# Performance work log

Measured on AMD Instinct MI355X. Metric: run time of the kernel, lower is better.

## Reference

```python
import jax, jax.numpy as jnp
import numpy as np

B, S, HID = 2, 2048, 768
NH, HD = 12, 64  # num heads, head dim


def setup_inputs() -> dict:
    key = jax.random.key(0)
    ks = jax.random.split(key, 10)
    scale = 0.02
    return {
        "hidden_states": jax.random.normal(ks[0], (B, S, HID), jnp.float32),
        "rel_pos": jax.random.normal(ks[1], (B, NH, S, S), jnp.float32),
        "rel_2d_pos": jax.random.normal(ks[2], (B, NH, S, S), jnp.float32),
        "attention_mask": jax.random.randint(ks[3], (B, 1, S, S), 0, 2, jnp.int32),
        "Wq": jax.random.normal(ks[4], (HID, HID), jnp.float32) * scale,
        "bq": jnp.zeros((HID,), jnp.float32),
        "Wk": jax.random.normal(ks[5], (HID, HID), jnp.float32) * scale,
        "bk": jnp.zeros((HID,), jnp.float32),
        "Wv": jax.random.normal(ks[6], (HID, HID), jnp.float32) * scale,
        "bv": jnp.zeros((HID,), jnp.float32),
    }


def _heads(x):
    # [B,S,HID] -> [B,NH,S,HD]
    return x.reshape(B, S, NH, HD).transpose(0, 2, 1, 3)


def reference(hidden_states, rel_pos, rel_2d_pos, attention_mask, Wq, bq, Wk, bk, Wv, bv):
    q = _heads(hidden_states @ Wq.T + bq) / jnp.sqrt(jnp.asarray(HD, hidden_states.dtype))
    k = _heads(hidden_states @ Wk.T + bk)
    v = _heads(hidden_states @ Wv.T + bv)
    scores = jnp.einsum('bhsd,bhtd->bhst', q, k)
    scores = scores + rel_pos + rel_2d_pos
    scores = jnp.where(attention_mask.astype(bool), jnp.finfo(jnp.float32).min, scores.astype(jnp.float32))
    probs = jax.nn.softmax(scores, axis=-1).astype(v.dtype)
    ctx = jnp.einsum('bhst,bhtd->bhsd', probs, v)
    return ctx.transpose(0, 2, 1, 3).reshape(B, S, HID)
```

## Files before the change

### kernel.cpp

```cpp
#include <hip/hip_runtime.h>

#define B_ 2
#define S_ 2048
#define HID_ 768
#define NH_ 12
#define HD_ 64
#define NSPLIT 2
#define KSPAN (S_ / NSPLIT)
#define NROWS (B_ * NH_ * S_)

typedef unsigned short u16;
typedef __attribute__((ext_vector_type(8))) short bf16x8;
typedef __attribute__((ext_vector_type(4))) float f32x4;

static __device__ inline u16 f2bf(float f) {
    union { float f; unsigned u; } v; v.f = f;
    unsigned r = v.u + 0x7fffu + ((v.u >> 16) & 1u);
    return (u16)(r >> 16);
}

#define LDS_BARRIER() asm volatile("s_waitcnt lgkmcnt(0)\n\ts_barrier" ::: "memory")

__global__ void cast_bf16(const float* __restrict__ src, u16* __restrict__ dst, int n) {
    int i = (blockIdx.x * blockDim.x + threadIdx.x) * 4;
    if (i < n) {
        float4 v = *(const float4*)(src + i);
        unsigned lo = (unsigned)f2bf(v.x) | ((unsigned)f2bf(v.y) << 16);
        unsigned hi = (unsigned)f2bf(v.z) | ((unsigned)f2bf(v.w) << 16);
        uint2 o; o.x = lo; o.y = hi;
        *(uint2*)(dst + i) = o;
    }
}

__global__ __launch_bounds__(256) void qkv_gemm(
    const u16* __restrict__ hsb, const u16* __restrict__ wcat,
    const float* __restrict__ bq, const float* __restrict__ bk, const float* __restrict__ bv,
    u16* __restrict__ Qg, u16* __restrict__ Kg, u16* __restrict__ Vtg)
{
    __shared__ u16 As[64 * 40];
    __shared__ u16 Bs[64 * 40];
    __shared__ u16 Vs[64 * 72];

    const int m0 = blockIdx.x * 64;
    const int n0 = blockIdx.y * 64;
    const int tid = threadIdx.x;
    const int wave = tid >> 6, lane = tid & 63;
    const int l = lane & 15, quad = lane >> 4;

    f32x4 acc[4];
#pragma unroll
    for (int t = 0; t < 4; t++) acc[t] = (f32x4){0.f, 0.f, 0.f, 0.f};

    const int srow = tid >> 2;
    const int skg = (tid & 3) * 8;

    for (int k0 = 0; k0 < HID_; k0 += 32) {
        *(int4*)(&As[srow * 40 + skg]) = *(const int4*)(&hsb[(size_t)(m0 + srow) * HID_ + k0 + skg]);
        *(int4*)(&Bs[srow * 40 + skg]) = *(const int4*)(&wcat[(size_t)(n0 + srow) * HID_ + k0 + skg]);
        __syncthreads();
        bf16x8 a = *(const bf16x8*)(&As[(wave * 16 + l) * 40 + quad * 8]);
#pragma unroll
        for (int t = 0; t < 4; t++) {
            bf16x8 b = *(const bf16x8*)(&Bs[(t * 16 + l) * 40 + quad * 8]);
            acc[t] = __builtin_amdgcn_mfma_f32_16x16x32_bf16(a, b, acc[t], 0, 0, 0);
        }
        __syncthreads();
    }

    const int proj = n0 / HID_;
    const int cbase = n0 - proj * HID_;
    const int h = cbase >> 6;
    const int bidx = m0 >> 11;
    const int srow0 = m0 & (S_ - 1);
    const float* bias = (proj == 0) ? bq : ((proj == 1) ? bk : bv);

    if (proj < 2) {
        u16* dst = (proj == 0) ? Qg : Kg;
        const float sc = (proj == 0) ? 0.125f : 1.0f;
#pragma unroll
        for (int t = 0; t < 4; t++) {
            const int d = t * 16 + l;
            const float bb = bias[cbase + d];
#pragma unroll
            for (int rr = 0; rr < 4; rr++) {
                int s = srow0 + wave * 16 + quad * 4 + rr;
                float v = (acc[t][rr] + bb) * sc;
                dst[(((size_t)bidx * NH_ + h) * S_ + s) * HD_ + d] = f2bf(v);
            }
        }
    } else {
#pragma unroll
        for (int t = 0; t < 4; t++) {
            const int d = t * 16 + l;
            const float bb = bias[cbase + d];
#pragma unroll
            for (int rr = 0; rr < 4; rr++) {
                int sl = wave * 16 + quad * 4 + rr;
                Vs[d * 72 + sl] = f2bf(acc[t][rr] + bb);
            }
        }
        __syncthreads();
        const int drow = tid >> 2;
        const int sseg = (tid & 3) * 16;
        size_t base = (((size_t)bidx * NH_ + h) * HD_ + drow) * S_ + srow0 + sseg;
        *(int4*)(&Vtg[base])     = *(const int4*)(&Vs[drow * 72 + sseg]);
        *(int4*)(&Vtg[base + 8]) = *(const int4*)(&Vs[drow * 72 + sseg + 8]);
    }
}

__global__ __launch_bounds__(256) void attn(
    const u16* __restrict__ Qg, const u16* __restrict__ Kg, const u16* __restrict__ Vtg,
    const float* __restrict__ rel, const float* __restrict__ rel2,
    const int* __restrict__ mask,
    float* __restrict__ Opart, float* __restrict__ Mpart, float* __restrict__ Lpart)
{
    __shared__ u16 Ks[64 * 72];
    __shared__ u16 Vts[64 * 72];
    __shared__ u16 Ps[4 * 16 * 72];

    const int q0 = blockIdx.x * 64;
    const int h = blockIdx.y;
    const int b = blockIdx.z / NSPLIT;
    const int split = blockIdx.z - b * NSPLIT;
    const int tid = threadIdx.x;
    const int wave = tid >> 6, lane = tid & 63;
    const int l = lane & 15, quad = lane >> 4;
    const int bh = b * NH_ + h;
    const int kbase = split * KSPAN;
    const int kend = kbase + KSPAN;

    const float NEG = -3.4028234663852886e38f;

    bf16x8 qf[2];
    {
        const int qr = q0 + wave * 16 + l;
        qf[0] = *(const bf16x8*)(&Qg[((size_t)bh * S_ + qr) * HD_ + quad * 8]);
        qf[1] = *(const bf16x8*)(&Qg[((size_t)bh * S_ + qr) * HD_ + 32 + quad * 8]);
    }

    f32x4 o[4];
#pragma unroll
    for (int t = 0; t < 4; t++) o[t] = (f32x4){0.f, 0.f, 0.f, 0.f};
    float m_run = NEG, l_run = 0.f;

    const int srow = tid >> 2;
    const int sseg = (tid & 3) * 8;

    const int qrow = q0 + wave * 16 + l;
    const float* relR  = rel  + (size_t)bh * S_ * S_ + (size_t)qrow * S_;
    const float* rel2R = rel2 + (size_t)bh * S_ * S_ + (size_t)qrow * S_;
    const int*   maskR = mask + (size_t)b * S_ * S_ + (size_t)qrow * S_;

    float4 pr1[4], pr2[4];
    int4 pmk[4];
#pragma unroll
    for (int t = 0; t < 4; t++) {
        const int c = kbase + t * 16 + quad * 4;
        pr1[t] = *(const float4*)(relR + c);
        pr2[t] = *(const float4*)(rel2R + c);
        pmk[t] = *(const int4*)(maskR + c);
    }

    for (int k0 = kbase; k0 < kend; k0 += 64) {
        size_t kg = ((size_t)bh * S_ + k0 + srow) * HD_;
        int4 ka = *(const int4*)(&Kg[kg + sseg]);
        int4 kb = *(const int4*)(&Kg[kg + 32 + sseg]);
        size_t vg = ((size_t)bh * HD_ + srow) * S_ + k0;
        int4 va = *(const int4*)(&Vtg[vg + sseg]);
        int4 vb = *(const int4*)(&Vtg[vg + 32 + sseg]);

        f32x4 sacc[4];
#pragma unroll
        for (int t = 0; t < 4; t++) {
            sacc[t][0] = pmk[t].x ? NEG : pr1[t].x + pr2[t].x;
            sacc[t][1] = pmk[t].y ? NEG : pr1[t].y + pr2[t].y;
            sacc[t][2] = pmk[t].z ? NEG : pr1[t].z + pr2[t].z;
            sacc[t][3] = pmk[t].w ? NEG : pr1[t].w + pr2[t].w;
        }

        if (k0 + 64 < kend) {
#pragma unroll
            for (int t = 0; t < 4; t++) {
                const int c = k0 + 64 + t * 16 + quad * 4;
                pr1[t] = *(const float4*)(relR + c);
                pr2[t] = *(const float4*)(rel2R + c);
                pmk[t] = *(const int4*)(maskR + c);
            }
        }

        *(int4*)(&Ks[srow * 72 + sseg])       = ka;
        *(int4*)(&Ks[srow * 72 + 32 + sseg])  = kb;
        *(int4*)(&Vts[srow * 72 + sseg])      = va;
        *(int4*)(&Vts[srow * 72 + 32 + sseg]) = vb;
        LDS_BARRIER();

#pragma unroll
        for (int t = 0; t < 4; t++) {
            bf16x8 b0 = *(const bf16x8*)(&Ks[(t * 16 + l) * 72 + quad * 8]);
            sacc[t] = __builtin_amdgcn_mfma_f32_16x16x32_bf16(b0, qf[0], sacc[t], 0, 0, 0);
            bf16x8 b1 = *(const bf16x8*)(&Ks[(t * 16 + l) * 72 + 32 + quad * 8]);
            sacc[t] = __builtin_amdgcn_mfma_f32_16x16x32_bf16(b1, qf[1], sacc[t], 0, 0, 0);
        }

        float mx = NEG;
#pragma unroll
        for (int t = 0; t < 4; t++)
#pragma unroll
            for (int rr = 0; rr < 4; rr++) mx = fmaxf(mx, sacc[t][rr]);
        mx = fmaxf(mx, __shfl_xor(mx, 16, 64));
        mx = fmaxf(mx, __shfl_xor(mx, 32, 64));
        float mnew = fmaxf(m_run, mx);
        float alpha = __expf(m_run - mnew);
        float rs = 0.f;
#pragma unroll
        for (int t = 0; t < 4; t++)
#pragma unroll
            for (int rr = 0; rr < 4; rr++) {
                float p = __expf(sacc[t][rr] - mnew);
                sacc[t][rr] = p;
                rs += p;
            }
        rs += __shfl_xor(rs, 16, 64);
        rs += __shfl_xor(rs, 32, 64);
        l_run = l_run * alpha + rs;
        m_run = mnew;

        float av[4];
#pragma unroll
        for (int rr = 0; rr < 4; rr++) av[rr] = __shfl(alpha, quad * 4 + rr, 64);
#pragma unroll
        for (int dt = 0; dt < 4; dt++)
#pragma unroll
            for (int rr = 0; rr < 4; rr++) o[dt][rr] *= av[rr];

#pragma unroll
        for (int t = 0; t < 4; t++) {
            unsigned p01 = (unsigned)f2bf(sacc[t][0]) | ((unsigned)f2bf(sacc[t][1]) << 16);
            unsigned p23 = (unsigned)f2bf(sacc[t][2]) | ((unsigned)f2bf(sacc[t][3]) << 16);
            uint2 pw; pw.x = p01; pw.y = p23;
            *(uint2*)(&Ps[(wave * 16 + l) * 72 + t * 16 + quad * 4]) = pw;
        }

        bf16x8 pa0 = *(const bf16x8*)(&Ps[(wave * 16 + l) * 72 + quad * 8]);
        bf16x8 pa1 = *(const bf16x8*)(&Ps[(wave * 16 + l) * 72 + 32 + quad * 8]);
#pragma unroll
        for (int dt = 0; dt < 4; dt++) {
            bf16x8 v0 = *(const bf16x8*)(&Vts[(dt * 16 + l) * 72 + quad * 8]);
            o[dt] = __builtin_amdgcn_mfma_f32_16x16x32_bf16(pa0, v0, o[dt], 0, 0, 0);
            bf16x8 v1 = *(const bf16x8*)(&Vts[(dt * 16 + l) * 72 + 32 + quad * 8]);
            o[dt] = __builtin_amdgcn_mfma_f32_16x16x32_bf16(pa1, v1, o[dt], 0, 0, 0);
        }
        LDS_BARRIER();
    }

    float* Op = Opart + (((size_t)split * B_ * NH_ + bh) * S_ + q0) * HD_;
#pragma unroll
    for (int dt = 0; dt < 4; dt++) {
#pragma unroll
        for (int rr = 0; rr < 4; rr++) {
            const int row = wave * 16 + quad * 4 + rr;
            Op[(size_t)row * HD_ + dt * 16 + l] = o[dt][rr];
        }
    }
    if (quad == 0) {
        const size_t mi = ((size_t)split * B_ * NH_ + bh) * S_ + q0 + wave * 16 + l;
        Mpart[mi] = m_run;
        Lpart[mi] = l_run;
    }
}

__global__ __launch_bounds__(256) void combine(
    const float* __restrict__ Op, const float* __restrict__ Mp, const float* __restrict__ Lp,
    float* __restrict__ out)
{
    const int idx = blockIdx.x * 256 + threadIdx.x;
    const int r = idx >> 4;
    const int dseg = (idx & 15) * 4;
    const float m0 = Mp[r], m1 = Mp[NROWS + r];
    const float l0 = Lp[r], l1 = Lp[NROWS + r];
    const float m = fmaxf(m0, m1);
    const float a0 = __expf(m0 - m), a1 = __expf(m1 - m);
    const float inv = 1.0f / (l0 * a0 + l1 * a1);
    const float4 o0 = *(const float4*)(Op + (size_t)r * HD_ + dseg);
    const float4 o1 = *(const float4*)(Op + ((size_t)NROWS + r) * HD_ + dseg);
    float4 res;
    res.x = (o0.x * a0 + o1.x * a1) * inv;
    res.y = (o0.y * a0 + o1.y * a1) * inv;
    res.z = (o0.z * a0 + o1.z * a1) * inv;
    res.w = (o0.w * a0 + o1.w * a1) * inv;
    const int bh_ = r >> 11;
    const int s = r & (S_ - 1);
    const int b = bh_ / NH_;
    const int h = bh_ - b * NH_;
    *(float4*)(out + ((size_t)(b * S_ + s)) * HID_ + h * HD_ + dseg) = res;
}

extern "C" void kernel_launch(void* const* d_in, const int* in_sizes, int n_in,
                              void* d_out, int out_size, void* d_ws, size_t ws_size,
                              hipStream_t stream) {
    const float* hs   = (const float*)d_in[0];
    const float* rel  = (const float*)d_in[1];
    const float* rel2 = (const float*)d_in[2];
    const int*   mask = (const int*)d_in[3];
    const float* Wq = (const float*)d_in[4];
    const float* bq = (const float*)d_in[5];
    const float* Wk = (const float*)d_in[6];
    const float* bk = (const float*)d_in[7];
    const float* Wv = (const float*)d_in[8];
    const float* bv = (const float*)d_in[9];
    float* out = (float*)d_out;

    char* ws = (char*)d_ws;
    u16* hsb   = (u16*)(ws);
    u16* wcat  = (u16*)(ws + 6291456);
    u16* Qg    = (u16*)(ws + 9830400);
    u16* Kg    = (u16*)(ws + 16121856);
    u16* Vtg   = (u16*)(ws + 22413312);
    float* Opart = (float*)(ws + 28704768);
    float* Mpart = (float*)(ws + 53870592);
    float* Lpart = (float*)(ws + 54263808);

    cast_bf16<<<3072, 256, 0, stream>>>(hs, hsb, B_ * S_ * HID_);
    cast_bf16<<<576, 256, 0, stream>>>(Wq, wcat,             HID_ * HID_);
    cast_bf16<<<576, 256, 0, stream>>>(Wk, wcat + HID_ * HID_,     HID_ * HID_);
    cast_bf16<<<576, 256, 0, stream>>>(Wv, wcat + 2 * HID_ * HID_, HID_ * HID_);

    qkv_gemm<<<dim3(64, 36), 256, 0, stream>>>(hsb, wcat, bq, bk, bv, Qg, Kg, Vtg);

    attn<<<dim3(S_ / 64, NH_, B_ * NSPLIT), 256, 0, stream>>>(
        Qg, Kg, Vtg, rel, rel2, mask, Opart, Mpart, Lpart);

    combine<<<(NROWS * 16) / 256, 256, 0, stream>>>(Opart, Mpart, Lpart, out);
}
```

Measured before the change: 905.7 us.

## Coalesce rel_pos/mask loads by row-major lane mapping and redistribute via shuffles

Changes how each wave loads the rel_pos, rel_2d_pos and mask tiles. Each group of four lanes now reads a contiguous 64-element row segment, replacing the scattered per-lane row reads. The values are then moved into the MFMA accumulator layout with cross-lane shuffles. This also removes the register prefetch of the next tile, so the loads are issued in the same iteration and are exposed, in exchange for better coalescing and fewer live registers.

```diff
diff --git a/kernel.cpp b/kernel.cpp
--- a/kernel.cpp
+++ b/kernel.cpp
@@ -146,20 +146,13 @@
     const int srow = tid >> 2;
     const int sseg = (tid & 3) * 8;
 
-    const int qrow = q0 + wave * 16 + l;
-    const float* relR  = rel  + (size_t)bh * S_ * S_ + (size_t)qrow * S_;
-    const float* rel2R = rel2 + (size_t)bh * S_ * S_ + (size_t)qrow * S_;
-    const int*   maskR = mask + (size_t)b * S_ * S_ + (size_t)qrow * S_;
-
-    float4 pr1[4], pr2[4];
-    int4 pmk[4];
-#pragma unroll
-    for (int t = 0; t < 4; t++) {
-        const int c = kbase + t * 16 + quad * 4;
-        pr1[t] = *(const float4*)(relR + c);
-        pr2[t] = *(const float4*)(rel2R + c);
-        pmk[t] = *(const int4*)(maskR + c);
-    }
+    const int rsub = lane >> 2;
+    const int rcol = (lane & 3) * 4;
+    const int rrow = q0 + wave * 16 + rsub;
+    const float* relS  = rel  + (size_t)bh * S_ * S_ + (size_t)rrow * S_;
+    const float* rel2S = rel2 + (size_t)bh * S_ * S_ + (size_t)rrow * S_;
+    const int*   maskS = mask + (size_t)b  * S_ * S_ + (size_t)rrow * S_;
+    const int srcLane = 4 * l + quad;
 
     for (int k0 = kbase; k0 < kend; k0 += 64) {
         size_t kg = ((size_t)bh * S_ + k0 + srow) * HD_;
@@ -169,29 +162,39 @@
         int4 va = *(const int4*)(&Vtg[vg + sseg]);
         int4 vb = *(const int4*)(&Vtg[vg + 32 + sseg]);
 
-        f32x4 sacc[4];
-#pragma unroll
-        for (int t = 0; t < 4; t++) {
-            sacc[t][0] = pmk[t].x ? NEG : pr1[t].x + pr2[t].x;
-            sacc[t][1] = pmk[t].y ? NEG : pr1[t].y + pr2[t].y;
-            sacc[t][2] = pmk[t].z ? NEG : pr1[t].z + pr2[t].z;
-            sacc[t][3] = pmk[t].w ? NEG : pr1[t].w + pr2[t].w;
-        }
-
-        if (k0 + 64 < kend) {
-#pragma unroll
-            for (int t = 0; t < 4; t++) {
-                const int c = k0 + 64 + t * 16 + quad * 4;
-                pr1[t] = *(const float4*)(relR + c);
-                pr2[t] = *(const float4*)(rel2R + c);
-                pmk[t] = *(const int4*)(maskR + c);
-            }
+        float4 r[4], s2[4];
+        int4 mk[4];
+#pragma unroll
+        for (int i = 0; i < 4; i++) {
+            const int c = k0 + rcol + i * 16;
+            r[i]  = *(const float4*)(relS + c);
+            s2[i] = *(const float4*)(rel2S + c);
+            mk[i] = *(const int4*)(maskS + c);
         }
 
         *(int4*)(&Ks[srow * 72 + sseg])       = ka;
         *(int4*)(&Ks[srow * 72 + 32 + sseg])  = kb;
         *(int4*)(&Vts[srow * 72 + sseg])      = va;
         *(int4*)(&Vts[srow * 72 + 32 + sseg]) = vb;
+
+        f32x4 ss[4];
+#pragma unroll
+        for (int i = 0; i < 4; i++) {
+            ss[i][0] = mk[i].x ? NEG : r[i].x + s2[i].x;
+            ss[i][1] = mk[i].y ? NEG : r[i].y + s2[i].y;
+            ss[i][2] = mk[i].z ? NEG : r[i].z + s2[i].z;
+            ss[i][3] = mk[i].w ? NEG : r[i].w + s2[i].w;
+        }
+
+        f32x4 sacc[4];
+#pragma unroll
+        for (int t = 0; t < 4; t++) {
+            sacc[t][0] = __shfl(ss[t][0], srcLane, 64);
+            sacc[t][1] = __shfl(ss[t][1], srcLane, 64);
+            sacc[t][2] = __shfl(ss[t][2], srcLane, 64);
+            sacc[t][3] = __shfl(ss[t][3], srcLane, 64);
+        }
+
         LDS_BARRIER();
 
 #pragma unroll
```

Result: faster. 880.2 us (-2.8%).

## Bit-pack mask, stage rel-pos sums in LDS, shuffle P into MFMA operands

Applied to the files above, without the earlier changes.

A new pre-pass kernel packs the int32 attention mask into 64-bit ballot words, so the attention kernel reads one bit per element instead of an int32 per head. The attention kernel now loads rel_pos and rel_2d_pos with row-wise coalesced float4 loads in 256-column chunks. It adds them, applies the mask, and stores the result as bf16 in a large LDS buffer that each 64-key tile reads back. The P-to-MFMA-operand conversion now uses cross-lane shuffles instead of an LDS round trip. This is meant to cut global memory traffic and uncoalesced access, but the larger LDS footprint may lower occupancy and the bf16 bias sum adds rounding error.

```diff
diff --git a/kernel.cpp b/kernel.cpp
--- a/kernel.cpp
+++ b/kernel.cpp
@@ -10,6 +10,7 @@
 #define NROWS (B_ * NH_ * S_)
 
 typedef unsigned short u16;
+typedef unsigned int uint;
 typedef __attribute__((ext_vector_type(8))) short bf16x8;
 typedef __attribute__((ext_vector_type(4))) float f32x4;
 
@@ -17,6 +18,9 @@
     union { float f; unsigned u; } v; v.f = f;
     unsigned r = v.u + 0x7fffu + ((v.u >> 16) & 1u);
     return (u16)(r >> 16);
+}
+static __device__ inline float bf2f(uint u) {
+    union { unsigned u; float f; } v; v.u = u << 16; return v.f;
 }
 
 #define LDS_BARRIER() asm volatile("s_waitcnt lgkmcnt(0)\n\ts_barrier" ::: "memory")
@@ -32,6 +36,14 @@
     }
 }
 
+__global__ __launch_bounds__(256) void pack_mask(const int* __restrict__ m, uint2* __restrict__ out) {
+    const int w = blockIdx.x * 4 + (threadIdx.x >> 6);
+    const int lane = threadIdx.x & 63;
+    const int v = m[(size_t)w * 64 + lane];
+    unsigned long long bl = __ballot(v != 0);
+    if (lane == 0) { uint2 o; o.x = (uint)bl; o.y = (uint)(bl >> 32); out[w] = o; }
+}
+
 __global__ __launch_bounds__(256) void qkv_gemm(
     const u16* __restrict__ hsb, const u16* __restrict__ wcat,
     const float* __restrict__ bq, const float* __restrict__ bk, const float* __restrict__ bv,
@@ -111,12 +123,12 @@
 __global__ __launch_bounds__(256) void attn(
     const u16* __restrict__ Qg, const u16* __restrict__ Kg, const u16* __restrict__ Vtg,
     const float* __restrict__ rel, const float* __restrict__ rel2,
-    const int* __restrict__ mask,
+    const uint2* __restrict__ maskb,
     float* __restrict__ Opart, float* __restrict__ Mpart, float* __restrict__ Lpart)
 {
+    __shared__ u16 relsum[64 * 268];
     __shared__ u16 Ks[64 * 72];
     __shared__ u16 Vts[64 * 72];
-    __shared__ u16 Ps[4 * 16 * 72];
 
     const int q0 = blockIdx.x * 64;
     const int h = blockIdx.y;
@@ -127,15 +139,14 @@
     const int l = lane & 15, quad = lane >> 4;
     const int bh = b * NH_ + h;
     const int kbase = split * KSPAN;
-    const int kend = kbase + KSPAN;
 
     const float NEG = -3.4028234663852886e38f;
 
-    bf16x8 qf[2];
+    bf16x8 qf0, qf1;
     {
         const int qr = q0 + wave * 16 + l;
-        qf[0] = *(const bf16x8*)(&Qg[((size_t)bh * S_ + qr) * HD_ + quad * 8]);
-        qf[1] = *(const bf16x8*)(&Qg[((size_t)bh * S_ + qr) * HD_ + 32 + quad * 8]);
+        qf0 = *(const bf16x8*)(&Qg[((size_t)bh * S_ + qr) * HD_ + quad * 8]);
+        qf1 = *(const bf16x8*)(&Qg[((size_t)bh * S_ + qr) * HD_ + 32 + quad * 8]);
     }
 
     f32x4 o[4];
@@ -146,111 +157,142 @@
     const int srow = tid >> 2;
     const int sseg = (tid & 3) * 8;
 
-    const int qrow = q0 + wave * 16 + l;
-    const float* relR  = rel  + (size_t)bh * S_ * S_ + (size_t)qrow * S_;
-    const float* rel2R = rel2 + (size_t)bh * S_ * S_ + (size_t)qrow * S_;
-    const int*   maskR = mask + (size_t)b * S_ * S_ + (size_t)qrow * S_;
-
-    float4 pr1[4], pr2[4];
-    int4 pmk[4];
-#pragma unroll
-    for (int t = 0; t < 4; t++) {
-        const int c = kbase + t * 16 + quad * 4;
-        pr1[t] = *(const float4*)(relR + c);
-        pr2[t] = *(const float4*)(rel2R + c);
-        pmk[t] = *(const int4*)(maskR + c);
-    }
-
-    for (int k0 = kbase; k0 < kend; k0 += 64) {
-        size_t kg = ((size_t)bh * S_ + k0 + srow) * HD_;
-        int4 ka = *(const int4*)(&Kg[kg + sseg]);
-        int4 kb = *(const int4*)(&Kg[kg + 32 + sseg]);
-        size_t vg = ((size_t)bh * HD_ + srow) * S_ + k0;
-        int4 va = *(const int4*)(&Vtg[vg + sseg]);
-        int4 vb = *(const int4*)(&Vtg[vg + 32 + sseg]);
-
-        f32x4 sacc[4];
+    const float* relQ  = rel  + (size_t)bh * S_ * S_ + (size_t)q0 * S_;
+    const float* rel2Q = rel2 + (size_t)bh * S_ * S_ + (size_t)q0 * S_;
+    const uint2* mQ    = maskb + (size_t)(b * S_ + q0) * (S_ / 64);
+
+    const int A16a = l + 32 * (quad & 1);
+    const int A16b = A16a + 16;
+
+    for (int ss = 0; ss < KSPAN; ss += 256) {
+        const int c0 = kbase + ss;
+
+#pragma unroll
+        for (int g = 0; g < 2; g++) {
+            float4 xa[8], xb[8];
+            uint2  xm[8];
+#pragma unroll
+            for (int r = 0; r < 8; r++) {
+                const int rowl = wave * 16 + g * 8 + r;
+                xa[r] = *(const float4*)(relQ  + (size_t)rowl * S_ + c0 + 4 * lane);
+                xb[r] = *(const float4*)(rel2Q + (size_t)rowl * S_ + c0 + 4 * lane);
+                xm[r] = mQ[(size_t)rowl * (S_ / 64) + (c0 >> 6) + (lane >> 4)];
+            }
+#pragma unroll
+            for (int r = 0; r < 8; r++) {
+                const int rowl = wave * 16 + g * 8 + r;
+                const uint wsel = (lane & 8) ? xm[r].y : xm[r].x;
+                const uint nib = (wsel >> ((lane & 7) * 4)) & 0xF;
+                const u16 NEGB = (u16)0xFF7F;
+                u16 e0 = (nib & 1) ? NEGB : f2bf(xa[r].x + xb[r].x);
+                u16 e1 = (nib & 2) ? NEGB : f2bf(xa[r].y + xb[r].y);
+                u16 e2 = (nib & 4) ? NEGB : f2bf(xa[r].z + xb[r].z);
+                u16 e3 = (nib & 8) ? NEGB : f2bf(xa[r].w + xb[r].w);
+                uint2 pw; pw.x = (uint)e0 | ((uint)e1 << 16); pw.y = (uint)e2 | ((uint)e3 << 16);
+                *(uint2*)(&relsum[rowl * 268 + 4 * lane]) = pw;
+            }
+        }
+
 #pragma unroll
         for (int t = 0; t < 4; t++) {
-            sacc[t][0] = pmk[t].x ? NEG : pr1[t].x + pr2[t].x;
-            sacc[t][1] = pmk[t].y ? NEG : pr1[t].y + pr2[t].y;
-            sacc[t][2] = pmk[t].z ? NEG : pr1[t].z + pr2[t].z;
-            sacc[t][3] = pmk[t].w ? NEG : pr1[t].w + pr2[t].w;
-        }
-
-        if (k0 + 64 < kend) {
-#pragma unroll
-            for (int t = 0; t < 4; t++) {
-                const int c = k0 + 64 + t * 16 + quad * 4;
-                pr1[t] = *(const float4*)(relR + c);
-                pr2[t] = *(const float4*)(rel2R + c);
-                pmk[t] = *(const int4*)(maskR + c);
-            }
-        }
-
-        *(int4*)(&Ks[srow * 72 + sseg])       = ka;
-        *(int4*)(&Ks[srow * 72 + 32 + sseg])  = kb;
-        *(int4*)(&Vts[srow * 72 + sseg])      = va;
-        *(int4*)(&Vts[srow * 72 + 32 + sseg]) = vb;
-        LDS_BARRIER();
-
-#pragma unroll
-        for (int t = 0; t < 4; t++) {
-            bf16x8 b0 = *(const bf16x8*)(&Ks[(t * 16 + l) * 72 + quad * 8]);
-            sacc[t] = __builtin_amdgcn_mfma_f32_16x16x32_bf16(b0, qf[0], sacc[t], 0, 0, 0);
-            bf16x8 b1 = *(const bf16x8*)(&Ks[(t * 16 + l) * 72 + 32 + quad * 8]);
-            sacc[t] = __builtin_amdgcn_mfma_f32_16x16x32_bf16(b1, qf[1], sacc[t], 0, 0, 0);
-        }
-
-        float mx = NEG;
-#pragma unroll
-        for (int t = 0; t < 4; t++)
-#pragma unroll
-            for (int rr = 0; rr < 4; rr++) mx = fmaxf(mx, sacc[t][rr]);
-        mx = fmaxf(mx, __shfl_xor(mx, 16, 64));
-        mx = fmaxf(mx, __shfl_xor(mx, 32, 64));
-        float mnew = fmaxf(m_run, mx);
-        float alpha = __expf(m_run - mnew);
-        float rs = 0.f;
-#pragma unroll
-        for (int t = 0; t < 4; t++)
-#pragma unroll
-            for (int rr = 0; rr < 4; rr++) {
-                float p = __expf(sacc[t][rr] - mnew);
-                sacc[t][rr] = p;
-                rs += p;
-            }
-        rs += __shfl_xor(rs, 16, 64);
-        rs += __shfl_xor(rs, 32, 64);
-        l_run = l_run * alpha + rs;
-        m_run = mnew;
-
-        float av[4];
-#pragma unroll
-        for (int rr = 0; rr < 4; rr++) av[rr] = __shfl(alpha, quad * 4 + rr, 64);
-#pragma unroll
-        for (int dt = 0; dt < 4; dt++)
-#pragma unroll
-            for (int rr = 0; rr < 4; rr++) o[dt][rr] *= av[rr];
-
-#pragma unroll
-        for (int t = 0; t < 4; t++) {
-            unsigned p01 = (unsigned)f2bf(sacc[t][0]) | ((unsigned)f2bf(sacc[t][1]) << 16);
-            unsigned p23 = (unsigned)f2bf(sacc[t][2]) | ((unsigned)f2bf(sacc[t][3]) << 16);
-            uint2 pw; pw.x = p01; pw.y = p23;
-            *(uint2*)(&Ps[(wave * 16 + l) * 72 + t * 16 + quad * 4]) = pw;
-        }
-
-        bf16x8 pa0 = *(const bf16x8*)(&Ps[(wave * 16 + l) * 72 + quad * 8]);
-        bf16x8 pa1 = *(const bf16x8*)(&Ps[(wave * 16 + l) * 72 + 32 + quad * 8]);
-#pragma unroll
-        for (int dt = 0; dt < 4; dt++) {
-            bf16x8 v0 = *(const bf16x8*)(&Vts[(dt * 16 + l) * 72 + quad * 8]);
-            o[dt] = __builtin_amdgcn_mfma_f32_16x16x32_bf16(pa0, v0, o[dt], 0, 0, 0);
-            bf16x8 v1 = *(const bf16x8*)(&Vts[(dt * 16 + l) * 72 + 32 + quad * 8]);
-            o[dt] = __builtin_amdgcn_mfma_f32_16x16x32_bf16(pa1, v1, o[dt], 0, 0, 0);
-        }
-        LDS_BARRIER();
+            const int k0 = c0 + t * 64;
+
+            size_t kg = ((size_t)bh * S_ + k0 + srow) * HD_;
+            int4 ka = *(const int4*)(&Kg[kg + sseg]);
+            int4 kb = *(const int4*)(&Kg[kg + 32 + sseg]);
+            size_t vg = ((size_t)bh * HD_ + srow) * S_ + k0;
+            int4 va = *(const int4*)(&Vtg[vg + sseg]);
+            int4 vb = *(const int4*)(&Vtg[vg + 32 + sseg]);
+            *(int4*)(&Ks[srow * 72 + sseg])       = ka;
+            *(int4*)(&Ks[srow * 72 + 32 + sseg])  = kb;
+            *(int4*)(&Vts[srow * 72 + sseg])      = va;
+            *(int4*)(&Vts[srow * 72 + 32 + sseg]) = vb;
+            LDS_BARRIER();
+
+            f32x4 sacc[4];
+#pragma unroll
+            for (int tt = 0; tt < 4; tt++) {
+                uint2 rv = *(const uint2*)(&relsum[(wave * 16 + l) * 268 + ss - ss  + t * 64 + tt * 16 + quad * 4]);
+                sacc[tt][0] = bf2f(rv.x & 0xFFFFu);
+                sacc[tt][1] = bf2f(rv.x >> 16);
+                sacc[tt][2] = bf2f(rv.y & 0xFFFFu);
+                sacc[tt][3] = bf2f(rv.y >> 16);
+            }
+
+#pragma unroll
+            for (int tt = 0; tt < 4; tt++) {
+                bf16x8 b0 = *(const bf16x8*)(&Ks[(tt * 16 + l) * 72 + quad * 8]);
+                sacc[tt] = __builtin_amdgcn_mfma_f32_16x16x32_bf16(b0, qf0, sacc[tt], 0, 0, 0);
+                bf16x8 b1 = *(const bf16x8*)(&Ks[(tt * 16 + l) * 72 + 32 + quad * 8]);
+                sacc[tt] = __builtin_amdgcn_mfma_f32_16x16x32_bf16(b1, qf1, sacc[tt], 0, 0, 0);
+            }
+
+            float mx = NEG;
+#pragma unroll
+            for (int tt = 0; tt < 4; tt++)
+#pragma unroll
+                for (int rr = 0; rr < 4; rr++) mx = fmaxf(mx, sacc[tt][rr]);
+            mx = fmaxf(mx, __shfl_xor(mx, 16, 64));
+            mx = fmaxf(mx, __shfl_xor(mx, 32, 64));
+            float mnew = fmaxf(m_run, mx);
+            float alpha = __expf(m_run - mnew);
+            float rs = 0.f;
+#pragma unroll
+            for (int tt = 0; tt < 4; tt++)
+#pragma unroll
+                for (int rr = 0; rr < 4; rr++) {
+                    float p = __expf(sacc[tt][rr] - mnew);
+                    sacc[tt][rr] = p;
+                    rs += p;
+                }
+            rs += __shfl_xor(rs, 16, 64);
+            rs += __shfl_xor(rs, 32, 64);
+            l_run = l_run * alpha + rs;
+            m_run = mnew;
+
+            float av[4];
+#pragma unroll
+            for (int rr = 0; rr < 4; rr++) av[rr] = __shfl(alpha, quad * 4 + rr, 64);
+#pragma unroll
+            for (int dt = 0; dt < 4; dt++)
+#pragma unroll
+                for (int rr = 0; rr < 4; rr++) o[dt][rr] *= av[rr];
+
+            uint pk0[4], pk1[4];
+#pragma unroll
+            for (int tt = 0; tt < 4; tt++) {
+                pk0[tt] = (uint)f2bf(sacc[tt][0]) | ((uint)f2bf(sacc[tt][1]) << 16);
+                pk1[tt] = (uint)f2bf(sacc[tt][2]) | ((uint)f2bf(sacc[tt][3]) << 16);
+            }
+            bf16x8 pa[2];
+#pragma unroll
+            for (int ks = 0; ks < 2; ks++) {
+                uint a0 = (uint)__shfl((int)pk0[2 * ks],     A16a, 64);
+                uint b0 = (uint)__shfl((int)pk0[2 * ks + 1], A16a, 64);
+                uint a1 = (uint)__shfl((int)pk1[2 * ks],     A16a, 64);
+                uint b1 = (uint)__shfl((int)pk1[2 * ks + 1], A16a, 64);
+                uint a2 = (uint)__shfl((int)pk0[2 * ks],     A16b, 64);
+                uint b2 = (uint)__shfl((int)pk0[2 * ks + 1], A16b, 64);
+                uint a3 = (uint)__shfl((int)pk1[2 * ks],     A16b, 64);
+                uint b3 = (uint)__shfl((int)pk1[2 * ks + 1], A16b, 64);
+                const bool hi = (quad & 2);
+                union { uint u[4]; bf16x8 v; } cv;
+                cv.u[0] = hi ? b0 : a0;
+                cv.u[1] = hi ? b1 : a1;
+                cv.u[2] = hi ? b2 : a2;
+                cv.u[3] = hi ? b3 : a3;
+                pa[ks] = cv.v;
+            }
+
+#pragma unroll
+            for (int dt = 0; dt < 4; dt++) {
+                bf16x8 v0 = *(const bf16x8*)(&Vts[(dt * 16 + l) * 72 + quad * 8]);
+                o[dt] = __builtin_amdgcn_mfma_f32_16x16x32_bf16(pa[0], v0, o[dt], 0, 0, 0);
+                bf16x8 v1 = *(const bf16x8*)(&Vts[(dt * 16 + l) * 72 + 32 + quad * 8]);
+                o[dt] = __builtin_amdgcn_mfma_f32_16x16x32_bf16(pa[1], v1, o[dt], 0, 0, 0);
+            }
+            LDS_BARRIER();
+        }
     }
 
     float* Op = Opart + (((size_t)split * B_ * NH_ + bh) * S_ + q0) * HD_;
@@ -319,16 +361,18 @@
     float* Opart = (float*)(ws + 28704768);
     float* Mpart = (float*)(ws + 53870592);
     float* Lpart = (float*)(ws + 54263808);
+    uint2* maskb = (uint2*)(ws + 54657024);
 
     cast_bf16<<<3072, 256, 0, stream>>>(hs, hsb, B_ * S_ * HID_);
     cast_bf16<<<576, 256, 0, stream>>>(Wq, wcat,             HID_ * HID_);
     cast_bf16<<<576, 256, 0, stream>>>(Wk, wcat + HID_ * HID_,     HID_ * HID_);
     cast_bf16<<<576, 256, 0, stream>>>(Wv, wcat + 2 * HID_ * HID_, HID_ * HID_);
+    pack_mask<<<(B_ * S_ * S_ / 64) / 4, 256, 0, stream>>>(mask, maskb);
 
     qkv_gemm<<<dim3(64, 36), 256, 0, stream>>>(hsb, wcat, bq, bk, bv, Qg, Kg, Vtg);
 
     attn<<<dim3(S_ / 64, NH_, B_ * NSPLIT), 256, 0, stream>>>(
-        Qg, Kg, Vtg, rel, rel2, mask, Opart, Mpart, Lpart);
+        Qg, Kg, Vtg, rel, rel2, maskb, Opart, Mpart, Lpart);
 
     combine<<<(NROWS * 16) / 256, 256, 0, stream>>>(Opart, Mpart, Lpart, out);
 }
```

Result: slower. 931.6 us (+2.9%).
